# Performance work log

Measured on AMD Instinct MI355X. Metric: run time of the kernel, lower is better.

The kernel has to match this reference:

```python
import jax, jax.numpy as jnp
import numpy as np

N_NODES = 20000
N_EDGES = 320000
IN_CH = 512
HEADS = 4
OUT_CH = 128
NEG_SLOPE = 0.2  # PyG GATConv default leaky_relu slope


def setup_inputs() -> dict:
    key = jax.random.key(0)
    k1, k2, k3, k4, k5 = jax.random.split(key, 5)
    x = jax.random.normal(k1, (N_NODES, IN_CH), dtype=jnp.float32)
    edge_index = jax.random.randint(k2, (2, N_EDGES), 0, N_NODES, dtype=jnp.int64)
    # Learned parameters (glorot-ish scaling)
    W = jax.random.normal(k3, (IN_CH, HEADS * OUT_CH), dtype=jnp.float32) * np.float32(1.0 / np.sqrt(IN_CH))
    att_src = jax.random.normal(k4, (HEADS, OUT_CH), dtype=jnp.float32) * np.float32(0.1)
    att_dst = jax.random.normal(k5, (HEADS, OUT_CH), dtype=jnp.float32) * np.float32(0.1)
    bias = jnp.zeros((OUT_CH,), dtype=jnp.float32)
    return {"x": x, "W": W, "att_src": att_src, "att_dst": att_dst, "bias": bias, "edge_index": edge_index}


def reference(x, W, att_src, att_dst, bias, edge_index):
    N = x.shape[0]
    H, C = att_src.shape
    # add self-loops (PyG GATConv default add_self_loops=True)
    loop = jnp.arange(N, dtype=edge_index.dtype)
    ei = jnp.concatenate([edge_index, jnp.stack([loop, loop])], axis=1)
    src, dst = ei[0], ei[1]
    # linear projection: [N, H, C]
    xl = (x @ W).reshape(N, H, C)
    # per-node attention halves: [N, H]
    a_s = jnp.einsum('nhc,hc->nh', xl, att_src)
    a_d = jnp.einsum('nhc,hc->nh', xl, att_dst)
    # per-edge logits + segment softmax over incoming edges (grouped by dst)
    alpha = jax.nn.leaky_relu(a_s[src] + a_d[dst], negative_slope=NEG_SLOPE)  # [E, H]
    amax = jax.ops.segment_max(alpha, dst, num_segments=N)  # every node has a self-loop -> no empty segments
    ae = jnp.exp(alpha - amax[dst])
    denom = jax.ops.segment_sum(ae, dst, num_segments=N)
    alpha = ae / (denom[dst] + 1e-16)
    # weighted scatter-add of source features: [N, H, C]
    out = jax.ops.segment_sum(alpha[:, :, None] * xl[src], dst, num_segments=N)
    # concat=False -> mean over heads, then bias [C]
    out = out.mean(axis=1) + bias
    return jax.nn.elu(out)
```

## Files before the change

kernel.cpp:

```cpp
#include <hip/hip_runtime.h>
#include <math.h>

#define N_NODES 20000
#define N_PAD 20096
#define N_EDGES 320000
#define IN_CH 512
#define HEADS 4
#define OUT_CH 128
#define HC 512
#define NEG_SLOPE 0.2f
#define BUCKET 96

#define CVX_BLOCKS 5024
#define CVW_BLOCKS 64
#define CNT_BLOCKS 1250

#define GEMM_WGS 628
#define GEMM_XQ 78
#define GEMM_XR 4

typedef __attribute__((ext_vector_type(8))) short short8;
typedef __attribute__((ext_vector_type(4))) float float4v;

__device__ __forceinline__ int detect_is64(const int* __restrict__ ei32) {
    int is64 = 1;
    #pragma unroll
    for (int i = 0; i < 32; i++) is64 &= (ei32[2 * i + 1] == 0);
    return is64;
}

__device__ __forceinline__ int edge_at(const void* ei, int is64, long long idx) {
    return is64 ? (int)((const long long*)ei)[idx] : ((const int*)ei)[idx];
}

__device__ __forceinline__ unsigned short f2bf(float f) {
    union { float f; unsigned u; } v; v.f = f;
    unsigned r = v.u + 0x7fffu + ((v.u >> 16) & 1u);
    return (unsigned short)(r >> 16);
}

__device__ __forceinline__ void bf8_decode(uint4 r, float* f) {
    f[0] = __uint_as_float(r.x << 16); f[1] = __uint_as_float(r.x & 0xffff0000u);
    f[2] = __uint_as_float(r.y << 16); f[3] = __uint_as_float(r.y & 0xffff0000u);
    f[4] = __uint_as_float(r.z << 16); f[5] = __uint_as_float(r.z & 0xffff0000u);
    f[6] = __uint_as_float(r.w << 16); f[7] = __uint_as_float(r.w & 0xffff0000u);
}

__device__ __forceinline__ float leaky(float t) { return t > 0.f ? t : NEG_SLOPE * t; }

__global__ __launch_bounds__(256) void fusedA_kernel(const float* __restrict__ x,
                                                     const float* __restrict__ W,
                                                     unsigned short* __restrict__ xb,
                                                     unsigned short* __restrict__ Wt,
                                                     const void* __restrict__ ei,
                                                     int* __restrict__ counts,
                                                     int* __restrict__ sorted_src) {
    __shared__ float tile[64][65];
    int b = blockIdx.x;
    if (b < CVX_BLOCKS) {
        size_t i = ((size_t)b * 256 + threadIdx.x) * 8;
        unsigned short o[8];
        if (i < (size_t)N_NODES * IN_CH) {
            float4 f0 = *(const float4*)&x[i];
            float4 f1 = *(const float4*)&x[i + 4];
            o[0] = f2bf(f0.x); o[1] = f2bf(f0.y); o[2] = f2bf(f0.z); o[3] = f2bf(f0.w);
            o[4] = f2bf(f1.x); o[5] = f2bf(f1.y); o[6] = f2bf(f1.z); o[7] = f2bf(f1.w);
        } else {
            for (int k = 0; k < 8; k++) o[k] = 0;
        }
        *(short8*)&xb[i] = *(short8*)o;
    } else if (b < CVX_BLOCKS + CVW_BLOCKS) {
        int idx = b - CVX_BLOCKS;
        int k0 = (idx & 7) * 64, n0 = (idx >> 3) * 64;
        int t = threadIdx.x, r = t >> 6, c = t & 63;
        for (int rr = r; rr < 64; rr += 4)
            tile[rr][c] = W[(size_t)(k0 + rr) * HC + n0 + c];
        __syncthreads();
        for (int rr = r; rr < 64; rr += 4)
            Wt[(size_t)(n0 + rr) * IN_CH + k0 + c] = f2bf(tile[c][rr]);
    } else {
        int is64 = detect_is64((const int*)ei);
        int e = (b - CVX_BLOCKS - CVW_BLOCKS) * 256 + threadIdx.x;
        if (e < N_EDGES) {
            int dst = edge_at(ei, is64, (long long)N_EDGES + e);
            int src = edge_at(ei, is64, e);
            int p = atomicAdd(&counts[dst], 1);
            sorted_src[dst * BUCKET + p] = src;
        }
    }
}

__global__ __launch_bounds__(256, 3) void gemm_kernel(const unsigned short* __restrict__ A,
                                                      const unsigned short* __restrict__ Bt,
                                                      unsigned short* __restrict__ Cb,
                                                      const float* __restrict__ att_s,
                                                      const float* __restrict__ att_d,
                                                      float* __restrict__ a_s,
                                                      float* __restrict__ a_d) {
    __shared__ __align__(16) unsigned short As[2][64 * 32];
    __shared__ __align__(16) unsigned short Bs[2][256 * 32];

    const int bid = blockIdx.x;
    const int xcd = bid & 7, rank = bid >> 3;
    const int w = (xcd < GEMM_XR) ? xcd * (GEMM_XQ + 1) + rank
                                  : GEMM_XR * (GEMM_XQ + 1) + (xcd - GEMM_XR) * GEMM_XQ + rank;
    const int bm = (w >> 1) * 64;
    const int bn = (w & 1) * 256;

    const int t = threadIdx.x;
    const int wv = t >> 6, lane = t & 63;
    const int wm = wv & 1, wn = wv >> 1;
    const int lm = lane & 15, lk = lane >> 4;

    float4v acc[2][8];
    #pragma unroll
    for (int i = 0; i < 2; i++)
        #pragma unroll
        for (int j = 0; j < 8; j++) acc[i][j] = (float4v){0.f, 0.f, 0.f, 0.f};

    const int srow = t >> 2;
    const int sk   = ((t & 3) ^ ((t >> 3) & 3)) * 8;
    const int swr  = (lk ^ ((lm >> 1) & 3)) * 8;

#define GEMM_STAGE(buf, kof)                                                                   \
    {                                                                                          \
        const unsigned short* gA = A + (size_t)(bm + srow) * IN_CH + (kof) + sk;               \
        __builtin_amdgcn_global_load_lds((const __attribute__((address_space(1))) void*)gA,    \
            (__attribute__((address_space(3))) void*)&As[buf][t * 8], 16, 0, 0);               \
        _Pragma("unroll")                                                                      \
        for (int q = 0; q < 4; q++) {                                                          \
            const unsigned short* gB = Bt + (size_t)(bn + q * 64 + srow) * IN_CH + (kof) + sk; \
            __builtin_amdgcn_global_load_lds((const __attribute__((address_space(1))) void*)gB,\
                (__attribute__((address_space(3))) void*)&Bs[buf][q * 2048 + t * 8], 16, 0, 0);\
        }                                                                                      \
    }

    GEMM_STAGE(0, 0);
    #pragma unroll
    for (int kk = 0; kk < 16; ++kk) {
        const int cur = kk & 1;
        if (kk < 15) {
            GEMM_STAGE(cur ^ 1, (kk + 1) * 32);
            asm volatile("s_waitcnt vmcnt(5)" ::: "memory");
        } else {
            asm volatile("s_waitcnt vmcnt(0)" ::: "memory");
        }
        __builtin_amdgcn_s_barrier();
        __builtin_amdgcn_sched_barrier(0);

        short8 af[2], bf[8];
        #pragma unroll
        for (int i = 0; i < 2; i++)
            af[i] = *(const short8*)&As[cur][(wm * 32 + i * 16 + lm) * 32 + swr];
        #pragma unroll
        for (int j = 0; j < 8; j++)
            bf[j] = *(const short8*)&Bs[cur][(wn * 128 + j * 16 + lm) * 32 + swr];
        #pragma unroll
        for (int i = 0; i < 2; i++)
            #pragma unroll
            for (int j = 0; j < 8; j++)
                acc[i][j] = __builtin_amdgcn_mfma_f32_16x16x32_bf16(af[i], bf[j], acc[i][j], 0, 0, 0);

        __builtin_amdgcn_sched_barrier(0);
        __builtin_amdgcn_s_barrier();
    }
#undef GEMM_STAGE

    #pragma unroll
    for (int i = 0; i < 2; i++) {
        #pragma unroll
        for (int r = 0; r < 4; r++) {
            int row = bm + wm * 32 + i * 16 + lk * 4 + r;
            if (row < N_NODES) {
                #pragma unroll
                for (int j = 0; j < 8; j++) {
                    int col = bn + wn * 128 + j * 16 + lm;
                    Cb[(size_t)row * HC + col] = f2bf(acc[i][j][r]);
                }
            }
        }
    }

    const int h = (bn >> 7) + wn;
    float as_w[8], ad_w[8];
    #pragma unroll
    for (int j = 0; j < 8; j++) {
        int col = h * 128 + j * 16 + lm;
        as_w[j] = att_s[col];
        ad_w[j] = att_d[col];
    }
    float ps[2][4], pd[2][4];
    #pragma unroll
    for (int i = 0; i < 2; i++)
        #pragma unroll
        for (int r = 0; r < 4; r++) {
            float s = 0.f, d = 0.f;
            #pragma unroll
            for (int j = 0; j < 8; j++) { s += acc[i][j][r] * as_w[j]; d += acc[i][j][r] * ad_w[j]; }
            ps[i][r] = s; pd[i][r] = d;
        }
    #pragma unroll
    for (int off = 1; off < 16; off <<= 1) {
        #pragma unroll
        for (int i = 0; i < 2; i++)
            #pragma unroll
            for (int r = 0; r < 4; r++) {
                ps[i][r] += __shfl_xor(ps[i][r], off, 64);
                pd[i][r] += __shfl_xor(pd[i][r], off, 64);
            }
    }
    if (lm == 0) {
        #pragma unroll
        for (int i = 0; i < 2; i++)
            #pragma unroll
            for (int r = 0; r < 4; r++) {
                int row = bm + wm * 32 + i * 16 + lk * 4 + r;
                if (row < N_NODES) {
                    a_s[row * 4 + h] = ps[i][r];
                    a_d[row * 4 + h] = pd[i][r];
                }
            }
    }
}

__global__ __launch_bounds__(256) void gather_kernel(const unsigned short* __restrict__ xlb,
                                                     const float* __restrict__ a_s,
                                                     const float* __restrict__ a_d,
                                                     const int* __restrict__ counts,
                                                     const int* __restrict__ sorted_src,
                                                     const float* __restrict__ bias,
                                                     float* __restrict__ out) {
    __shared__ float cl[2][64][9];
    int wv = threadIdx.x >> 6;
    int nib = wv >> 1;
    int sub = wv & 1;
    int node = blockIdx.x * 2 + nib;
    int lane = threadIdx.x & 63;
    int hd = lane >> 4;
    int beg = node * BUCKET, end = beg + counts[node];

    const float ad_hd = a_d[node * 4 + hd];
    const unsigned short* xrow = xlb + lane * 8;
    float acc[8] = {0, 0, 0, 0, 0, 0, 0, 0};
    float denom = 0.f;

    int c0 = beg + sub * 4;
    int s0 = 0, s1 = 0, s2 = 0, s3 = 0;
    float w0 = 0.f, w1 = 0.f, w2 = 0.f, w3 = 0.f;
    if (c0 < end) {
        int lim = end - 1;
        int i1 = c0 + 1 > lim ? lim : c0 + 1;
        int i2 = c0 + 2 > lim ? lim : c0 + 2;
        int i3 = c0 + 3 > lim ? lim : c0 + 3;
        s0 = sorted_src[c0]; s1 = sorted_src[i1]; s2 = sorted_src[i2]; s3 = sorted_src[i3];
        w0 = __expf(leaky(a_s[s0 * 4 + hd] + ad_hd));
        w1 = (c0 + 1 < end) ? __expf(leaky(a_s[s1 * 4 + hd] + ad_hd)) : 0.f;
        w2 = (c0 + 2 < end) ? __expf(leaky(a_s[s2 * 4 + hd] + ad_hd)) : 0.f;
        w3 = (c0 + 3 < end) ? __expf(leaky(a_s[s3 * 4 + hd] + ad_hd)) : 0.f;
    }

    if (sub == 0) {
        float w = __expf(leaky(a_s[node * 4 + hd] + ad_hd));
        denom = w;
        uint4 r = *(const uint4*)(xrow + (size_t)node * HC);
        float f[8];
        bf8_decode(r, f);
        #pragma unroll
        for (int k = 0; k < 8; k++) acc[k] = w * f[k];
    }

    for (; c0 < end; c0 += 8) {
        uint4 r0 = *(const uint4*)(xrow + (size_t)s0 * HC);
        uint4 r1 = *(const uint4*)(xrow + (size_t)s1 * HC);
        uint4 r2 = *(const uint4*)(xrow + (size_t)s2 * HC);
        uint4 r3 = *(const uint4*)(xrow + (size_t)s3 * HC);

        int c1 = c0 + 8;
        int n0 = 0, n1 = 0, n2 = 0, n3 = 0;
        float v0 = 0.f, v1 = 0.f, v2 = 0.f, v3 = 0.f;
        if (c1 < end) {
            int lim = end - 1;
            int i1 = c1 + 1 > lim ? lim : c1 + 1;
            int i2 = c1 + 2 > lim ? lim : c1 + 2;
            int i3 = c1 + 3 > lim ? lim : c1 + 3;
            n0 = sorted_src[c1]; n1 = sorted_src[i1]; n2 = sorted_src[i2]; n3 = sorted_src[i3];
            v0 = __expf(leaky(a_s[n0 * 4 + hd] + ad_hd));
            v1 = (c1 + 1 < end) ? __expf(leaky(a_s[n1 * 4 + hd] + ad_hd)) : 0.f;
            v2 = (c1 + 2 < end) ? __expf(leaky(a_s[n2 * 4 + hd] + ad_hd)) : 0.f;
            v3 = (c1 + 3 < end) ? __expf(leaky(a_s[n3 * 4 + hd] + ad_hd)) : 0.f;
        }

        denom += (w0 + w1) + (w2 + w3);
        float f0[8], f1[8], f2[8], f3[8];
        bf8_decode(r0, f0);
        bf8_decode(r1, f1);
        bf8_decode(r2, f2);
        bf8_decode(r3, f3);
        #pragma unroll
        for (int k = 0; k < 8; k++)
            acc[k] += (w0 * f0[k] + w1 * f1[k]) + (w2 * f2[k] + w3 * f3[k]);

        s0 = n0; s1 = n1; s2 = n2; s3 = n3;
        w0 = v0; w1 = v1; w2 = v2; w3 = v3;
    }

    if (sub == 1) {
        #pragma unroll
        for (int k = 0; k < 8; k++) cl[nib][lane][k] = acc[k];
        cl[nib][lane][8] = denom;
    }
    __syncthreads();
    if (sub == 0) {
        #pragma unroll
        for (int k = 0; k < 8; k++) acc[k] += cl[nib][lane][k];
        denom += cl[nib][lane][8];

        float rd = 0.25f / (denom + 1e-16f);
        float v[8];
        #pragma unroll
        for (int k = 0; k < 8; k++) {
            float t = acc[k] * rd;
            t += __shfl_xor(t, 16, 64);
            t += __shfl_xor(t, 32, 64);
            v[k] = t;
        }
        if (hd == 0) {
            float4 b0 = *(const float4*)&bias[lane * 8];
            float4 b1 = *(const float4*)&bias[lane * 8 + 4];
            float o[8];
            o[0] = v[0] + b0.x; o[1] = v[1] + b0.y; o[2] = v[2] + b0.z; o[3] = v[3] + b0.w;
            o[4] = v[4] + b1.x; o[5] = v[5] + b1.y; o[6] = v[6] + b1.z; o[7] = v[7] + b1.w;
            #pragma unroll
            for (int k = 0; k < 8; k++) o[k] = o[k] > 0.f ? o[k] : expm1f(o[k]);
            *(float4*)&out[(size_t)node * OUT_CH + lane * 8]     = make_float4(o[0], o[1], o[2], o[3]);
            *(float4*)&out[(size_t)node * OUT_CH + lane * 8 + 4] = make_float4(o[4], o[5], o[6], o[7]);
        }
    }
}

extern "C" void kernel_launch(void* const* d_in, const int* in_sizes, int n_in,
                              void* d_out, int out_size, void* d_ws, size_t ws_size,
                              hipStream_t stream) {
    const float* x       = (const float*)d_in[0];
    const float* W       = (const float*)d_in[1];
    const float* att_src = (const float*)d_in[2];
    const float* att_dst = (const float*)d_in[3];
    const float* bias    = (const float*)d_in[4];
    const void*  ei      = d_in[5];
    float* out = (float*)d_out;

    char* ws = (char*)d_ws;
    size_t off = 0;
    unsigned short* xlb = (unsigned short*)(ws + off); off += (size_t)N_PAD * HC * sizeof(unsigned short);
    float* a_s     = (float*)(ws + off); off += (size_t)N_NODES * HEADS * sizeof(float);
    float* a_d     = (float*)(ws + off); off += (size_t)N_NODES * HEADS * sizeof(float);
    int* counts    = (int*)(ws + off);   off += (size_t)N_NODES * sizeof(int);
    off = (off + 15) & ~(size_t)15;
    int* sorted_src = (int*)(ws + off);  off += (size_t)N_NODES * BUCKET * sizeof(int);
    off = (off + 15) & ~(size_t)15;
    unsigned short* xb = (unsigned short*)(ws + off); off += (size_t)N_PAD * IN_CH * sizeof(unsigned short);
    unsigned short* Wt = (unsigned short*)(ws + off); off += (size_t)IN_CH * HC * sizeof(unsigned short);

    hipMemsetAsync(counts, 0, N_NODES * sizeof(int), stream);
    fusedA_kernel<<<CVX_BLOCKS + CVW_BLOCKS + CNT_BLOCKS, 256, 0, stream>>>(x, W, xb, Wt, ei, counts, sorted_src);
    gemm_kernel<<<GEMM_WGS, 256, 0, stream>>>(xb, Wt, xlb, att_src, att_dst, a_s, a_d);
    gather_kernel<<<N_NODES / 2, 256, 0, stream>>>(xlb, a_s, a_d, counts, sorted_src, bias, out);
}
```

Measured before the change: 180.7 us.

## Fuse fp32-to-bf16 conversion of x into GEMM A-tile loading

Removes the separate pass that converted x to a bf16 buffer. The GEMM now loads fp32 x directly into registers one stage ahead, converts to bf16, and writes the A tile to LDS itself, while B still uses direct global-to-LDS loads. This saves a full write and re-read of the bf16 copy of x. In exchange, x is read twice (once per N-half block) at fp32 width, and register conversion plus LDS stores are added to the GEMM's inner loop.

```diff
diff --git a/kernel.cpp b/kernel.cpp
--- a/kernel.cpp
+++ b/kernel.cpp
@@ -11,7 +11,6 @@
 #define NEG_SLOPE 0.2f
 #define BUCKET 96
 
-#define CVX_BLOCKS 5024
 #define CVW_BLOCKS 64
 #define CNT_BLOCKS 1250
 
@@ -48,29 +47,15 @@
 
 __device__ __forceinline__ float leaky(float t) { return t > 0.f ? t : NEG_SLOPE * t; }
 
-__global__ __launch_bounds__(256) void fusedA_kernel(const float* __restrict__ x,
-                                                     const float* __restrict__ W,
-                                                     unsigned short* __restrict__ xb,
+__global__ __launch_bounds__(256) void fusedA_kernel(const float* __restrict__ W,
                                                      unsigned short* __restrict__ Wt,
                                                      const void* __restrict__ ei,
                                                      int* __restrict__ counts,
                                                      int* __restrict__ sorted_src) {
     __shared__ float tile[64][65];
     int b = blockIdx.x;
-    if (b < CVX_BLOCKS) {
-        size_t i = ((size_t)b * 256 + threadIdx.x) * 8;
-        unsigned short o[8];
-        if (i < (size_t)N_NODES * IN_CH) {
-            float4 f0 = *(const float4*)&x[i];
-            float4 f1 = *(const float4*)&x[i + 4];
-            o[0] = f2bf(f0.x); o[1] = f2bf(f0.y); o[2] = f2bf(f0.z); o[3] = f2bf(f0.w);
-            o[4] = f2bf(f1.x); o[5] = f2bf(f1.y); o[6] = f2bf(f1.z); o[7] = f2bf(f1.w);
-        } else {
-            for (int k = 0; k < 8; k++) o[k] = 0;
-        }
-        *(short8*)&xb[i] = *(short8*)o;
-    } else if (b < CVX_BLOCKS + CVW_BLOCKS) {
-        int idx = b - CVX_BLOCKS;
+    if (b < CVW_BLOCKS) {
+        int idx = b;
         int k0 = (idx & 7) * 64, n0 = (idx >> 3) * 64;
         int t = threadIdx.x, r = t >> 6, c = t & 63;
         for (int rr = r; rr < 64; rr += 4)
@@ -80,7 +65,7 @@
             Wt[(size_t)(n0 + rr) * IN_CH + k0 + c] = f2bf(tile[c][rr]);
     } else {
         int is64 = detect_is64((const int*)ei);
-        int e = (b - CVX_BLOCKS - CVW_BLOCKS) * 256 + threadIdx.x;
+        int e = (b - CVW_BLOCKS) * 256 + threadIdx.x;
         if (e < N_EDGES) {
             int dst = edge_at(ei, is64, (long long)N_EDGES + e);
             int src = edge_at(ei, is64, e);
@@ -90,7 +75,7 @@
     }
 }
 
-__global__ __launch_bounds__(256, 3) void gemm_kernel(const unsigned short* __restrict__ A,
+__global__ __launch_bounds__(256, 3) void gemm_kernel(const float* __restrict__ X,
                                                       const unsigned short* __restrict__ Bt,
                                                       unsigned short* __restrict__ Cb,
                                                       const float* __restrict__ att_s,
@@ -122,11 +107,11 @@
     const int sk   = ((t & 3) ^ ((t >> 3) & 3)) * 8;
     const int swr  = (lk ^ ((lm >> 1) & 3)) * 8;
 
-#define GEMM_STAGE(buf, kof)                                                                   \
+    int agr = bm + srow; if (agr >= N_NODES) agr = N_NODES - 1;
+    const float* agp = X + (size_t)agr * IN_CH + sk;
+
+#define GEMM_STAGE_B(buf, kof)                                                                 \
     {                                                                                          \
-        const unsigned short* gA = A + (size_t)(bm + srow) * IN_CH + (kof) + sk;               \
-        __builtin_amdgcn_global_load_lds((const __attribute__((address_space(1))) void*)gA,    \
-            (__attribute__((address_space(3))) void*)&As[buf][t * 8], 16, 0, 0);               \
         _Pragma("unroll")                                                                      \
         for (int q = 0; q < 4; q++) {                                                          \
             const unsigned short* gB = Bt + (size_t)(bn + q * 64 + srow) * IN_CH + (kof) + sk; \
@@ -135,16 +120,32 @@
         }                                                                                      \
     }
 
-    GEMM_STAGE(0, 0);
+    float4 aA0, aB0, aA1, aB1;
+    aA0 = *(const float4*)(agp);
+    aB0 = *(const float4*)(agp + 4);
+    GEMM_STAGE_B(0, 0);
     #pragma unroll
     for (int kk = 0; kk < 16; ++kk) {
         const int cur = kk & 1;
         if (kk < 15) {
-            GEMM_STAGE(cur ^ 1, (kk + 1) * 32);
-            asm volatile("s_waitcnt vmcnt(5)" ::: "memory");
+            if (cur == 0) { aA1 = *(const float4*)(agp + (kk + 1) * 32);
+                            aB1 = *(const float4*)(agp + (kk + 1) * 32 + 4); }
+            else          { aA0 = *(const float4*)(agp + (kk + 1) * 32);
+                            aB0 = *(const float4*)(agp + (kk + 1) * 32 + 4); }
+            GEMM_STAGE_B(cur ^ 1, (kk + 1) * 32);
+            asm volatile("s_waitcnt vmcnt(6)" ::: "memory");
         } else {
             asm volatile("s_waitcnt vmcnt(0)" ::: "memory");
         }
+        {
+            float4 u = cur ? aA1 : aA0;
+            float4 v = cur ? aB1 : aB0;
+            unsigned short o[8];
+            o[0] = f2bf(u.x); o[1] = f2bf(u.y); o[2] = f2bf(u.z); o[3] = f2bf(u.w);
+            o[4] = f2bf(v.x); o[5] = f2bf(v.y); o[6] = f2bf(v.z); o[7] = f2bf(v.w);
+            *(short8*)&As[cur][t * 8] = *(short8*)o;
+        }
+        asm volatile("s_waitcnt lgkmcnt(0)" ::: "memory");
         __builtin_amdgcn_s_barrier();
         __builtin_amdgcn_sched_barrier(0);
 
@@ -164,7 +165,7 @@
         __builtin_amdgcn_sched_barrier(0);
         __builtin_amdgcn_s_barrier();
     }
-#undef GEMM_STAGE
+#undef GEMM_STAGE_B
 
     #pragma unroll
     for (int i = 0; i < 2; i++) {
@@ -358,11 +359,10 @@
     off = (off + 15) & ~(size_t)15;
     int* sorted_src = (int*)(ws + off);  off += (size_t)N_NODES * BUCKET * sizeof(int);
     off = (off + 15) & ~(size_t)15;
-    unsigned short* xb = (unsigned short*)(ws + off); off += (size_t)N_PAD * IN_CH * sizeof(unsigned short);
     unsigned short* Wt = (unsigned short*)(ws + off); off += (size_t)IN_CH * HC * sizeof(unsigned short);
 
     hipMemsetAsync(counts, 0, N_NODES * sizeof(int), stream);
-    fusedA_kernel<<<CVX_BLOCKS + CVW_BLOCKS + CNT_BLOCKS, 256, 0, stream>>>(x, W, xb, Wt, ei, counts, sorted_src);
-    gemm_kernel<<<GEMM_WGS, 256, 0, stream>>>(xb, Wt, xlb, att_src, att_dst, a_s, a_d);
+    fusedA_kernel<<<CVW_BLOCKS + CNT_BLOCKS, 256, 0, stream>>>(W, Wt, ei, counts, sorted_src);
+    gemm_kernel<<<GEMM_WGS, 256, 0, stream>>>(x, Wt, xlb, att_src, att_dst, a_s, a_d);
     gather_kernel<<<N_NODES / 2, 256, 0, stream>>>(xlb, a_s, a_d, counts, sorted_src, bias, out);
 }
```

After: 190.2 us. 1.05x slower.
